# Kernel optimization log

Measured on AMD Instinct MI355X. Metric: run time of the kernel, lower is better.

## Reference

```python
import jax, jax.numpy as jnp
import numpy as np

FEATURE_LENGTH = 512
EMBEDDING_DIM = 128
NUM_EMBEDDINGS = 2048
BATCH = 8192


def setup_inputs() -> dict:
    key = jax.random.key(0)
    k1, k2 = jax.random.split(key)
    feature = jax.random.normal(k1, (BATCH, FEATURE_LENGTH), dtype=jnp.float32)
    W = jax.random.normal(k2, (NUM_EMBEDDINGS, EMBEDDING_DIM), dtype=jnp.float32)
    return {"feature": feature, "W": W}


def reference(feature, W):
    # vqlizationWithLoss: nearest-codebook lookup + straight-through VQ loss
    f = feature.reshape(-1, EMBEDDING_DIM)  # [N, d], N = BATCH * FEATURE_LENGTH / d
    # expanded L2 distances: ||f||^2 - 2 f W^T + ||W||^2 (same argmin as cdist^2)
    d2 = (jnp.sum(f * f, axis=1, keepdims=True)
          - 2.0 * jnp.einsum('nd,kd->nk', f, W)
          + jnp.sum(W * W, axis=1))  # [N, K]
    j = jnp.argmin(d2, axis=1)  # [N]
    W_j = W[j]  # [N, d]
    out = W_j.reshape(-1, FEATURE_LENGTH)  # [BATCH, featureLength]
    f_sg = jax.lax.stop_gradient(f)
    W_j_sg = jax.lax.stop_gradient(W_j)
    loss = (jnp.sum((f - W_j_sg) ** 2, axis=1)
            + 0.25 * jnp.sum((f_sg - W_j) ** 2, axis=1))  # [N]
    loss = loss.reshape(-1, FEATURE_LENGTH // EMBEDDING_DIM).mean(axis=1)  # [BATCH]
    return loss, out
```

## Files before the change

### kernel.cpp

```cpp
#include <hip/hip_runtime.h>

#define D        128
#define KCODES   2048
#define NROWS    32768
#define BATCH    8192

typedef _Float16 f16x8 __attribute__((ext_vector_type(8)));
typedef float    f32x4 __attribute__((ext_vector_type(4)));

#define MFMA16(a, b, c) __builtin_amdgcn_mfma_f32_16x16x32_f16((a), (b), (c), 0, 0, 0)
#define INV2048 4.8828125e-4f

static __device__ __forceinline__ void gload16(const void* g, void* l) {
    __builtin_amdgcn_global_load_lds(
        (const __attribute__((address_space(1))) unsigned int*)g,
        (__attribute__((address_space(3))) unsigned int*)l, 16, 0, 0);
}

static __device__ __forceinline__ float dppmin16(float s) {
    int t;
    t = __builtin_amdgcn_update_dpp(0, __float_as_int(s), 0x121, 0xf, 0xf, true);
    s = fminf(s, __int_as_float(t));
    t = __builtin_amdgcn_update_dpp(0, __float_as_int(s), 0x122, 0xf, 0xf, true);
    s = fminf(s, __int_as_float(t));
    t = __builtin_amdgcn_update_dpp(0, __float_as_int(s), 0x124, 0xf, 0xf, true);
    s = fminf(s, __int_as_float(t));
    t = __builtin_amdgcn_update_dpp(0, __float_as_int(s), 0x128, 0xf, 0xf, true);
    s = fminf(s, __int_as_float(t));
    return s;
}

__global__ void wconv_kernel(const float* __restrict__ W,
                             _Float16* __restrict__ whf, _Float16* __restrict__ wlf,
                             float* __restrict__ wnorm) {
    int gid = blockIdx.x * 256 + threadIdx.x;
    int n = gid >> 4, s = gid & 15;
    const float4* src = (const float4*)(W + (size_t)n * D + s * 8);
    float4 a = src[0], b = src[1];
    float va[8] = {a.x, a.y, a.z, a.w, b.x, b.y, b.z, b.w};
    f16x8 hi, lo;
    float ss = 0.0f;
#pragma unroll
    for (int j = 0; j < 8; ++j) {
        _Float16 h = (_Float16)va[j];
        hi[j] = h;
        lo[j] = (_Float16)((va[j] - (float)h) * 2048.0f);
        ss += va[j] * va[j];
    }
    size_t idx = ((size_t)((n >> 4) * 4 + (s >> 2)) * 64 + (s & 3) * 16 + (n & 15));
    ((f16x8*)whf)[idx] = hi;
    ((f16x8*)wlf)[idx] = lo;
#pragma unroll
    for (int m = 1; m <= 8; m <<= 1) ss += __shfl_xor(ss, m);
    if (s == 0) wnorm[n] = ss;
}

__global__ void fconv_kernel(const float* __restrict__ f,
                             _Float16* __restrict__ fhf, _Float16* __restrict__ flf,
                             float* __restrict__ fnorm) {
    int gid = blockIdx.x * 256 + threadIdx.x;
    int n = gid >> 4, s = gid & 15;
    const float4* src = (const float4*)(f + (size_t)n * D + s * 8);
    float4 a = src[0], b = src[1];
    float va[8] = {a.x, a.y, a.z, a.w, b.x, b.y, b.z, b.w};
    f16x8 hi, lo;
    float ss = 0.0f;
#pragma unroll
    for (int j = 0; j < 8; ++j) {
        ss += va[j] * va[j];
        float x = -2.0f * va[j];
        _Float16 h = (_Float16)x;
        hi[j] = h;
        lo[j] = (_Float16)((x - (float)h) * 2048.0f);
    }
    size_t idx = ((size_t)((n >> 4) * 4 + (s >> 2)) * 64 + (s & 3) * 16 + (n & 15));
    ((f16x8*)fhf)[idx] = hi;
    ((f16x8*)flf)[idx] = lo;
#pragma unroll
    for (int m = 1; m <= 8; m <<= 1) ss += __shfl_xor(ss, m);
    if (s == 0) fnorm[n] = ss;
}

extern "C" __global__ void __launch_bounds__(512)
__attribute__((amdgpu_flat_work_group_size(512, 512)))
__attribute__((amdgpu_waves_per_eu(2, 2)))
vq_argmin(const _Float16* __restrict__ fhf, const _Float16* __restrict__ flf,
          const _Float16* __restrict__ whf, const _Float16* __restrict__ wlf,
          const float* __restrict__ wnorm,
          float* __restrict__ bsp, int* __restrict__ bcp) {
    extern __shared__ unsigned char lds[];

    const int b   = blockIdx.x;
    const int cb  = b & 3;
    const int rg  = b >> 2;
    const int tid = threadIdx.x;
    const int w   = tid >> 6, l = tid & 63;
    const int l15 = l & 15, lq = l >> 4;
    const int sw  = ((w >> 2) & 1) << 2;

    const char* fhB = (const char*)fhf + (size_t)rg * 131072;
    const char* flB = (const char*)flf + (size_t)rg * 131072;

#define STAGE(c) {                                                          \
        unsigned char* dB = lds + ((c) & 1) * 65536;                        \
        const char* sh = fhB + (size_t)(c) * 32768;                         \
        const char* sl = flB + (size_t)(c) * 32768;                         \
        gload16(sh + tid * 16,         dB + tid * 16);                      \
        gload16(sh + 8192  + tid * 16, dB + 8192  + tid * 16);              \
        gload16(sh + 16384 + tid * 16, dB + 16384 + tid * 16);              \
        gload16(sh + 24576 + tid * 16, dB + 24576 + tid * 16);              \
        gload16(sl + tid * 16,         dB + 32768 + tid * 16);              \
        gload16(sl + 8192  + tid * 16, dB + 40960 + tid * 16);              \
        gload16(sl + 16384 + tid * 16, dB + 49152 + tid * 16);              \
        gload16(sl + 24576 + tid * 16, dB + 57344 + tid * 16);              \
    }

    STAGE(0);

    f16x8 wh[4][4], wl[4][4];
    {
        const f16x8* whv = (const f16x8*)whf;
        const f16x8* wlv = (const f16x8*)wlf;
        const int n0 = cb * 32 + w * 4;
#pragma unroll
        for (int ct = 0; ct < 4; ++ct)
#pragma unroll
            for (int ks = 0; ks < 4; ++ks) {
                size_t idx = (size_t)((n0 + ct) * 4 + ks) * 64 + l;
                wh[ct][ks] = whv[idx];
                wl[ct][ks] = wlv[idx];
            }
    }
    float wv[4];
    unsigned mv[4];
#pragma unroll
    for (int ct = 0; ct < 4; ++ct) {
        wv[ct] = wnorm[cb * 512 + w * 64 + ct * 16 + l15];
        mv[ct] = (unsigned)(ct << 4) | (unsigned)l15;
    }

    __syncthreads();

    float* mrg = (float*)(lds + 131072);

#pragma unroll 1
    for (int c = 0; c < 4; ++c) {
        if (c < 3) STAGE(c + 1);
        const unsigned char* wb = lds + (c & 1) * 65536;

#pragma unroll 2
        for (int tlx = 0; tlx < 8; ++tlx) {
            const int tl = tlx ^ sw;
            f16x8 fhk[4], flk[4];
#pragma unroll
            for (int ks = 0; ks < 4; ++ks) {
                fhk[ks] = *(const f16x8*)(wb + ((tl * 4 + ks) << 10) + l * 16);
                flk[ks] = *(const f16x8*)(wb + 32768 + ((tl * 4 + ks) << 10) + l * 16);
            }

            f32x4 accC[4], accH[4];
#pragma unroll
            for (int ct = 0; ct < 4; ++ct)
#pragma unroll
                for (int r = 0; r < 4; ++r) { accC[ct][r] = 0.0f; accH[ct][r] = wv[ct]; }

#pragma unroll
            for (int ks = 0; ks < 4; ++ks) {
                __builtin_amdgcn_s_setprio(1);
#pragma unroll
                for (int ct = 0; ct < 4; ++ct)
                    accC[ct] = MFMA16(fhk[ks], wl[ct][ks], accC[ct]);
#pragma unroll
                for (int ct = 0; ct < 4; ++ct)
                    accH[ct] = MFMA16(fhk[ks], wh[ct][ks], accH[ct]);
#pragma unroll
                for (int ct = 0; ct < 4; ++ct)
                    accC[ct] = MFMA16(flk[ks], wh[ct][ks], accC[ct]);
                __builtin_amdgcn_s_setprio(0);
            }

            float bestR[4] = {3.4e38f, 3.4e38f, 3.4e38f, 3.4e38f};
#pragma unroll
            for (int ct = 0; ct < 4; ++ct)
#pragma unroll
                for (int r = 0; r < 4; ++r) {
                    float s = fmaf(accC[ct][r], INV2048, accH[ct][r]);
                    unsigned pk = (__float_as_uint(s) & 0xFFFFFFC0u) | mv[ct];
                    bestR[r] = fminf(bestR[r], __uint_as_float(pk));
                }
#pragma unroll
            for (int r = 0; r < 4; ++r) bestR[r] = dppmin16(bestR[r]);

            if (l15 == 0) {
                f32x4 v;
                v[0] = bestR[0]; v[1] = bestR[1]; v[2] = bestR[2]; v[3] = bestR[3];
                *(f32x4*)(mrg + w * 512 + c * 128 + tl * 16 + lq * 4) = v;
            }
        }
        asm volatile("s_waitcnt vmcnt(0)" ::: "memory");
        __builtin_amdgcn_s_barrier();
        asm volatile("" ::: "memory");
    }
#undef STAGE

    __syncthreads();
    {
        int row = tid;
        float s = mrg[row];
        int wBest = 0;
#pragma unroll
        for (int ww = 1; ww < 8; ++ww) {
            float s2 = mrg[ww * 512 + row];
            if (s2 < s) { s = s2; wBest = ww; }
        }
        unsigned bits = __float_as_uint(s);
        int code = cb * 512 + wBest * 64 + (int)((bits >> 4) & 3u) * 16 + (int)(bits & 15u);
        bsp[(size_t)cb * NROWS + rg * 512 + row] = s;
        bcp[(size_t)cb * NROWS + rg * 512 + row] = code;
    }
}

__global__ void gather_kernel(const float* __restrict__ W,
                              const float* __restrict__ fnorm,
                              const float* __restrict__ bsp, const int* __restrict__ bcp,
                              float* __restrict__ loss, float* __restrict__ outv) {
    int b  = blockIdx.x;
    int wv = threadIdx.x >> 6;
    int l  = threadIdx.x & 63;
    int n  = b * 4 + wv;
    float s; int c;
    if (l < 4) { s = bsp[(size_t)l * NROWS + n]; c = bcp[(size_t)l * NROWS + n]; }
    else       { s = 3.4e38f; c = 0x7FFFFFFF; }
#pragma unroll
    for (int msk = 1; msk <= 2; msk <<= 1) {
        float s2 = __shfl_xor(s, msk);
        int   c2 = __shfl_xor(c, msk);
        if (s2 < s || (s2 == s && c2 < c)) { s = s2; c = c2; }
    }
    int j = __shfl(c, 0);
    float smin = __shfl(s, 0);
    float2 wj = reinterpret_cast<const float2*>(W + (size_t)j * D)[l];
    reinterpret_cast<float2*>(outv + (size_t)n * D)[l] = wj;
    __shared__ float lsm[4];
    if (l == 0) lsm[wv] = smin + fnorm[n];
    __syncthreads();
    if (threadIdx.x == 0)
        loss[b] = 0.3125f * (lsm[0] + lsm[1] + lsm[2] + lsm[3]);
}

extern "C" void kernel_launch(void* const* d_in, const int* in_sizes, int n_in,
                              void* d_out, int out_size, void* d_ws, size_t ws_size,
                              hipStream_t stream) {
    const float* f = (const float*)d_in[0];
    const float* W = (const float*)d_in[1];

    float* loss = (float*)d_out;
    float* outv = (float*)d_out + BATCH;

    _Float16* fhf = (_Float16*)outv;
    _Float16* flf = (_Float16*)((char*)outv + 8388608);

    float*    wnorm = (float*)d_ws;
    _Float16* whf   = (_Float16*)((char*)d_ws + 8192);
    _Float16* wlf   = (_Float16*)((char*)d_ws + 532480);
    float*    bsp   = (float*)((char*)d_ws + 1056768);
    int*      bcp   = (int*)((char*)d_ws + 1581056);
    float*    fnorm = (float*)((char*)d_ws + 2105344);

    wconv_kernel<<<KCODES * 16 / 256, 256, 0, stream>>>(W, whf, wlf, wnorm);
    fconv_kernel<<<NROWS * 16 / 256, 256, 0, stream>>>(f, fhf, flf, fnorm);

    hipLaunchKernelGGL(vq_argmin, dim3(256), dim3(512), 147456, stream,
                       fhf, flf, whf, wlf, wnorm, bsp, bcp);

    gather_kernel<<<BATCH, 256, 0, stream>>>(W, fnorm, bsp, bcp, loss, outv);
}
```

Before: 67.61 us.

## Replace LDS double-buffered feature staging with direct global loads into registers

Removes the async global-to-LDS double-buffer pipeline for the fp16 hi/lo feature tiles. Each wave now loads its feature fragments straight from global memory into registers inside a flat 32-iteration loop, with no per-chunk barriers. Dynamic LDS drops from 144KB to a 16KB static merge buffer. All 8 waves read the same feature data redundantly through L1/L2, and latency hiding now depends on the compiler and occupancy instead of explicit prefetch.

```diff
diff --git a/kernel.cpp b/kernel.cpp
--- a/kernel.cpp
+++ b/kernel.cpp
@@ -10,12 +10,6 @@
 
 #define MFMA16(a, b, c) __builtin_amdgcn_mfma_f32_16x16x32_f16((a), (b), (c), 0, 0, 0)
 #define INV2048 4.8828125e-4f
-
-static __device__ __forceinline__ void gload16(const void* g, void* l) {
-    __builtin_amdgcn_global_load_lds(
-        (const __attribute__((address_space(1))) unsigned int*)g,
-        (__attribute__((address_space(3))) unsigned int*)l, 16, 0, 0);
-}
 
 static __device__ __forceinline__ float dppmin16(float s) {
     int t;
@@ -88,7 +82,7 @@
           const _Float16* __restrict__ whf, const _Float16* __restrict__ wlf,
           const float* __restrict__ wnorm,
           float* __restrict__ bsp, int* __restrict__ bcp) {
-    extern __shared__ unsigned char lds[];
+    __shared__ float mrg[8 * 512];
 
     const int b   = blockIdx.x;
     const int cb  = b & 3;
@@ -96,26 +90,6 @@
     const int tid = threadIdx.x;
     const int w   = tid >> 6, l = tid & 63;
     const int l15 = l & 15, lq = l >> 4;
-    const int sw  = ((w >> 2) & 1) << 2;
-
-    const char* fhB = (const char*)fhf + (size_t)rg * 131072;
-    const char* flB = (const char*)flf + (size_t)rg * 131072;
-
-#define STAGE(c) {                                                          \
-        unsigned char* dB = lds + ((c) & 1) * 65536;                        \
-        const char* sh = fhB + (size_t)(c) * 32768;                         \
-        const char* sl = flB + (size_t)(c) * 32768;                         \
-        gload16(sh + tid * 16,         dB + tid * 16);                      \
-        gload16(sh + 8192  + tid * 16, dB + 8192  + tid * 16);              \
-        gload16(sh + 16384 + tid * 16, dB + 16384 + tid * 16);              \
-        gload16(sh + 24576 + tid * 16, dB + 24576 + tid * 16);              \
-        gload16(sl + tid * 16,         dB + 32768 + tid * 16);              \
-        gload16(sl + 8192  + tid * 16, dB + 40960 + tid * 16);              \
-        gload16(sl + 16384 + tid * 16, dB + 49152 + tid * 16);              \
-        gload16(sl + 24576 + tid * 16, dB + 57344 + tid * 16);              \
-    }
-
-    STAGE(0);
 
     f16x8 wh[4][4], wl[4][4];
     {
@@ -139,69 +113,57 @@
         mv[ct] = (unsigned)(ct << 4) | (unsigned)l15;
     }
 
-    __syncthreads();
-
-    float* mrg = (float*)(lds + 131072);
-
-#pragma unroll 1
-    for (int c = 0; c < 4; ++c) {
-        if (c < 3) STAGE(c + 1);
-        const unsigned char* wb = lds + (c & 1) * 65536;
+    const f16x8* fhv = (const f16x8*)fhf + (size_t)rg * 8192;
+    const f16x8* flv = (const f16x8*)flf + (size_t)rg * 8192;
 
 #pragma unroll 2
-        for (int tlx = 0; tlx < 8; ++tlx) {
-            const int tl = tlx ^ sw;
-            f16x8 fhk[4], flk[4];
-#pragma unroll
-            for (int ks = 0; ks < 4; ++ks) {
-                fhk[ks] = *(const f16x8*)(wb + ((tl * 4 + ks) << 10) + l * 16);
-                flk[ks] = *(const f16x8*)(wb + 32768 + ((tl * 4 + ks) << 10) + l * 16);
+    for (int m = 0; m < 32; ++m) {
+        f16x8 fhk[4], flk[4];
+#pragma unroll
+        for (int ks = 0; ks < 4; ++ks) {
+            fhk[ks] = fhv[(m * 4 + ks) * 64 + l];
+            flk[ks] = flv[(m * 4 + ks) * 64 + l];
+        }
+
+        f32x4 accC[4], accH[4];
+#pragma unroll
+        for (int ct = 0; ct < 4; ++ct)
+#pragma unroll
+            for (int r = 0; r < 4; ++r) { accC[ct][r] = 0.0f; accH[ct][r] = wv[ct]; }
+
+#pragma unroll
+        for (int ks = 0; ks < 4; ++ks) {
+            __builtin_amdgcn_s_setprio(1);
+#pragma unroll
+            for (int ct = 0; ct < 4; ++ct)
+                accC[ct] = MFMA16(fhk[ks], wl[ct][ks], accC[ct]);
+#pragma unroll
+            for (int ct = 0; ct < 4; ++ct)
+                accH[ct] = MFMA16(fhk[ks], wh[ct][ks], accH[ct]);
+#pragma unroll
+            for (int ct = 0; ct < 4; ++ct)
+                accC[ct] = MFMA16(flk[ks], wh[ct][ks], accC[ct]);
+            __builtin_amdgcn_s_setprio(0);
+        }
+
+        float bestR[4] = {3.4e38f, 3.4e38f, 3.4e38f, 3.4e38f};
+#pragma unroll
+        for (int ct = 0; ct < 4; ++ct)
+#pragma unroll
+            for (int r = 0; r < 4; ++r) {
+                float s = fmaf(accC[ct][r], INV2048, accH[ct][r]);
+                unsigned pk = (__float_as_uint(s) & 0xFFFFFFC0u) | mv[ct];
+                bestR[r] = fminf(bestR[r], __uint_as_float(pk));
             }
-
-            f32x4 accC[4], accH[4];
-#pragma unroll
-            for (int ct = 0; ct < 4; ++ct)
-#pragma unroll
-                for (int r = 0; r < 4; ++r) { accC[ct][r] = 0.0f; accH[ct][r] = wv[ct]; }
-
-#pragma unroll
-            for (int ks = 0; ks < 4; ++ks) {
-                __builtin_amdgcn_s_setprio(1);
-#pragma unroll
-                for (int ct = 0; ct < 4; ++ct)
-                    accC[ct] = MFMA16(fhk[ks], wl[ct][ks], accC[ct]);
-#pragma unroll
-                for (int ct = 0; ct < 4; ++ct)
-                    accH[ct] = MFMA16(fhk[ks], wh[ct][ks], accH[ct]);
-#pragma unroll
-                for (int ct = 0; ct < 4; ++ct)
-                    accC[ct] = MFMA16(flk[ks], wh[ct][ks], accC[ct]);
-                __builtin_amdgcn_s_setprio(0);
-            }
-
-            float bestR[4] = {3.4e38f, 3.4e38f, 3.4e38f, 3.4e38f};
-#pragma unroll
-            for (int ct = 0; ct < 4; ++ct)
-#pragma unroll
-                for (int r = 0; r < 4; ++r) {
-                    float s = fmaf(accC[ct][r], INV2048, accH[ct][r]);
-                    unsigned pk = (__float_as_uint(s) & 0xFFFFFFC0u) | mv[ct];
-                    bestR[r] = fminf(bestR[r], __uint_as_float(pk));
-                }
-#pragma unroll
-            for (int r = 0; r < 4; ++r) bestR[r] = dppmin16(bestR[r]);
-
-            if (l15 == 0) {
-                f32x4 v;
-                v[0] = bestR[0]; v[1] = bestR[1]; v[2] = bestR[2]; v[3] = bestR[3];
-                *(f32x4*)(mrg + w * 512 + c * 128 + tl * 16 + lq * 4) = v;
-            }
-        }
-        asm volatile("s_waitcnt vmcnt(0)" ::: "memory");
-        __builtin_amdgcn_s_barrier();
-        asm volatile("" ::: "memory");
-    }
-#undef STAGE
+#pragma unroll
+        for (int r = 0; r < 4; ++r) bestR[r] = dppmin16(bestR[r]);
+
+        if (l15 == 0) {
+            f32x4 v;
+            v[0] = bestR[0]; v[1] = bestR[1]; v[2] = bestR[2]; v[3] = bestR[3];
+            *(f32x4*)(mrg + w * 512 + m * 16 + lq * 4) = v;
+        }
+    }
 
     __syncthreads();
     {
@@ -270,7 +232,7 @@
     wconv_kernel<<<KCODES * 16 / 256, 256, 0, stream>>>(W, whf, wlf, wnorm);
     fconv_kernel<<<NROWS * 16 / 256, 256, 0, stream>>>(f, fhf, flf, fnorm);
 
-    hipLaunchKernelGGL(vq_argmin, dim3(256), dim3(512), 147456, stream,
+    hipLaunchKernelGGL(vq_argmin, dim3(256), dim3(512), 0, stream,
                        fhf, flf, whf, wlf, wnorm, bsp, bcp);
 
     gather_kernel<<<BATCH, 256, 0, stream>>>(W, fnorm, bsp, bcp, loss, outv);
```

New measurement: 66.21 us. 1.02x faster.
